# Kernel tuning notes

Measured on AMD Instinct MI355X. Metric: run time of the kernel, lower is better.

The kernel has to match this reference:

```python
import jax, jax.numpy as jnp
import numpy as np

H = 10          # MPC horizon
DT = 0.1
MAX_V = 0.22
MAX_W = 2.8
N_RAYS = 36
LR_INNER = 0.2
N_ITERS = 15
B = 16384


def setup_inputs() -> dict:
    key = jax.random.key(0)
    ks = jax.random.split(key, 8)
    initial_state = jax.random.normal(ks[0], (B, 3), jnp.float32)
    scan_data = jax.random.uniform(ks[1], (B, N_RAYS), jnp.float32)
    target_pos = jax.random.normal(ks[2], (B, 2), jnp.float32)
    w_dist = jax.random.uniform(ks[3], (B, 1), jnp.float32)
    w_obs = jax.random.uniform(ks[4], (B, 1), jnp.float32)
    w_angle = jax.random.uniform(ks[5], (B, 1), jnp.float32)
    w_rv = jax.random.uniform(ks[6], (B, 1), jnp.float32)
    w_rw = jax.random.uniform(ks[7], (B, 1), jnp.float32)
    return {"initial_state": initial_state, "scan_data": scan_data,
            "target_pos": target_pos, "w_dist": w_dist, "w_obs": w_obs,
            "w_angle": w_angle, "w_rv": w_rv, "w_rw": w_rw}


def _rollout_cost(action_seq, initial_state, obstacles, target_pos,
                  w_dist, w_obs, w_angle, w_rv, w_rw):
    # action_seq: [B,H,2]; obstacles: [B,36,2]
    wd, wo, wa, wv, ww = (w.reshape(-1) for w in (w_dist, w_obs, w_angle, w_rv, w_rw))

    def step(carry, a_t):  # a_t: [B,2]
        state, cost = carry
        v = (jnp.tanh(a_t[:, 0]) + 1.0) * 0.5 * MAX_V
        w = jnp.tanh(a_t[:, 1]) * MAX_W
        x = state[:, 0] + v * jnp.cos(state[:, 2]) * DT
        y = state[:, 1] + v * jnp.sin(state[:, 2]) * DT
        yaw = state[:, 2] + w * DT
        state = jnp.stack([x, y, yaw], axis=1)
        pos = state[:, :2]
        dist_to_goal = jnp.linalg.norm(pos - target_pos, axis=1)
        tdir = target_pos - pos
        tang = jnp.arctan2(tdir[:, 1], tdir[:, 0])
        aerr = jnp.arctan2(jnp.sin(tang - yaw), jnp.cos(tang - yaw))
        d_obs = jnp.linalg.norm(pos[:, None, :] - obstacles, axis=2)  # [B,36]
        min_d = jnp.min(d_obs, axis=1)
        coll = jnp.maximum(0.4 - min_d, 0.0) ** 2
        cost = cost + (dist_to_goal ** 2 * wd * 10.0
                       + aerr ** 2 * wa * 5.0
                       + coll ** 2 * wo * 100.0
                       + v ** 2 * wv * 1.0
                       + w ** 2 * ww * 0.1)
        return (state, cost), None

    bsz = initial_state.shape[0]
    init = (initial_state, jnp.zeros((bsz,), initial_state.dtype))
    (_, cost), _ = jax.lax.scan(step, init, jnp.swapaxes(action_seq, 0, 1))
    return cost.mean()


def _mpc_forward(initial_state, scan_data, target_pos,
                 w_dist, w_obs, w_angle, w_rv, w_rw):
    bsz = initial_state.shape[0]
    angles = jnp.linspace(0.0, 2.0 * jnp.pi, N_RAYS).astype(scan_data.dtype)
    obstacles = jnp.stack([scan_data * jnp.cos(angles),
                           scan_data * jnp.sin(angles)], axis=2)  # [B,36,2]
    action_seq = jnp.zeros((bsz, H, 2), initial_state.dtype)
    cost_grad = jax.grad(_rollout_cost, argnums=0)
    for _ in range(N_ITERS):
        g = cost_grad(action_seq, initial_state, obstacles, target_pos,
                      w_dist, w_obs, w_angle, w_rv, w_rw)
        action_seq = action_seq - LR_INNER * g
    a0 = action_seq[:, 0, :]
    v = (jnp.tanh(a0[:, 0]) + 1.0) * 0.5 * MAX_V
    w = jnp.tanh(a0[:, 1]) * MAX_W
    return jnp.stack([v, w], axis=1)  # [B,2]


def reference(initial_state, scan_data, target_pos,
              w_dist, w_obs, w_angle, w_rv, w_rw):
    return _mpc_forward(initial_state, scan_data, target_pos,
                        w_dist, w_obs, w_angle, w_rv, w_rw)
```

## Files before the change

### kernel.cpp

```cpp
#include <hip/hip_runtime.h>

#define H 10
#define NIT 15
#define NPAIR 9

typedef float v2f __attribute__((ext_vector_type(2)));

__device__ __forceinline__ float rcp_fast(float x) { return __builtin_amdgcn_rcpf(x); }
__device__ __forceinline__ float rsq_fast(float x) { return __builtin_amdgcn_rsqf(x); }
__device__ __forceinline__ unsigned umin2(unsigned a, unsigned b) { return a < b ? a : b; }

__device__ __forceinline__ float fast_atan2f(float y, float x) {
    float ax = fabsf(x), ay = fabsf(y);
    float mx = fmaxf(ax, ay), mn = fminf(ax, ay);
    float z = mn * rcp_fast(mx);
    float z2 = z * z;
    float p = fmaf(z2, -0.01172120f, 0.05265332f);
    p = fmaf(z2, p, -0.11643287f);
    p = fmaf(z2, p, 0.19354346f);
    p = fmaf(z2, p, -0.33262347f);
    p = fmaf(z2, p, 0.99997726f);
    p = p * z;
    p = (ay > ax) ? (1.5707964f - p) : p;
    p = (x < 0.0f) ? (3.1415927f - p) : p;
    return copysignf(p, y);
}

__global__ __launch_bounds__(256) void mpc_kernel(
    const float* __restrict__ init_state,
    const float* __restrict__ scan,
    const float* __restrict__ target,
    const float* __restrict__ wdp, const float* __restrict__ wop,
    const float* __restrict__ wap, const float* __restrict__ wvp,
    const float* __restrict__ wwp,
    float* __restrict__ out, int B)
{
    constexpr float DTc  = 0.1f;
    constexpr float MAXV = 0.22f;
    constexpr float MAXW = 2.8f;
    constexpr float LRB  = 0.2f / 16384.0f;

    __shared__ v2f s_obs[64][37];

    const int tid  = threadIdx.x;
    const int g    = blockIdx.x * 256 + tid;
    const int b    = g >> 2;
    const int sub  = tid & 3;
    const int rpar = sub & 1;
    const int tpar = (sub >> 1) & 1;
    const int e    = tid >> 2;
    if (b >= B) return;

    v2f oxp[NPAIR], oyp[NPAIR];
    #pragma unroll
    for (int j = 0; j < NPAIR; ++j) {
        int rA = rpar + 4 * j;
        int rB = rA + 2;
        float angA = (float)rA * 0.17951958020513104f;
        float angB = (float)rB * 0.17951958020513104f;
        float sA, cA, sB, cB;
        __sincosf(angA, &sA, &cA);
        __sincosf(angB, &sB, &cB);
        float dA = scan[b * 36 + rA];
        float dB = scan[b * 36 + rB];
        oxp[j] = (v2f){dA * cA, dB * cB};
        oyp[j] = (v2f){dA * sA, dB * sB};
        float wx = tpar ? oxp[j].y : oxp[j].x;
        float wy = tpar ? oyp[j].y : oyp[j].x;
        s_obs[e][sub + 4 * j] = (v2f){wx, wy};
    }
    __syncthreads();

    const float x0   = init_state[b * 3 + 0];
    const float y0   = init_state[b * 3 + 1];
    const float yaw0 = init_state[b * 3 + 2];
    const float tx   = target[b * 2 + 0];
    const float ty   = target[b * 2 + 1];
    const float wd2 = wdp[b] * 20.0f;
    const float wo  = wop[b] * 100.0f;
    const float wa2 = wap[b] * 10.0f;
    const float wv2 = wvp[b] * 2.0f;
    const float ww2 = wwp[b] * 0.2f;

    float c0, s0;
    __sincosf(yaw0, &s0, &c0);

    float a[H][2];
    #pragma unroll
    for (int t = 0; t < H; ++t) { a[t][0] = 0.0f; a[t][1] = 0.0f; }

    for (int it = 0; it < NIT; ++it) {
        float vv[H], wl[H];
        #pragma unroll
        for (int t = 0; t < H; ++t) {
            float a0 = a[t][0], a1 = a[t][1];
            float t0 = a0 * fmaf(a0 * a0, -(1.0f / 3.0f), 1.0f);
            float t1 = a1 * fmaf(a1 * a1, -(1.0f / 3.0f), 1.0f);
            vv[t] = fmaf(t0, 0.5f * MAXV, 0.5f * MAXV);
            wl[t] = t1 * MAXW;
        }

        float cv[H], sv[H];
        float sx5[5] = {0}, sy5[5] = {0};
        float ca5[5] = {0}, sa5[5] = {0};
        float x = x0, y = y0, c = c0, s = s0;
        #pragma unroll
        for (int t = 0; t < H; ++t) {
            cv[t] = c; sv[t] = s;
            float v = vv[t], w = wl[t];
            x = fmaf(v * c, DTc, x);
            y = fmaf(v * s, DTc, y);
            float z  = w * DTc;
            float z2 = z * z;
            float sz = z * fmaf(z2, -0.16666667f, 1.0f);
            float cz = fmaf(z2, -0.5f, 1.0f);
            float cn = fmaf(c, cz, -s * sz);
            float sn = fmaf(s, cz,  c * sz);
            c = cn; s = sn;
            bool mine = ((t & 1) == tpar);
            int k = t >> 1;
            sx5[k] = mine ? x : sx5[k];
            sy5[k] = mine ? y : sy5[k];
            ca5[k] = mine ? c : ca5[k];
            sa5[k] = mine ? s : sa5[k];
        }

        float pgxE[5], pgxO[5], pgyE[5], pgyO[5], pcaE[5], pcaO[5];
        #pragma unroll
        for (int k = 0; k < 5; ++k) {
            const float xp = sx5[k], yp = sy5[k];
            const float cA = ca5[k], sA = sa5[k];

            float dx = tx - xp, dy = ty - yp;
            float nn = fmaf(dy, cA, -dx * sA);
            float dd = fmaf(dx, cA,  dy * sA);
            float aerr = fast_atan2f(nn, dd);
            float ca = wa2 * aerr;
            float r2 = fmaf(dx, dx, dy * dy);
            float cr = ca * rcp_fast(r2);
            float gx = fmaf(-wd2, dx,  cr * dy);
            float gy = fmaf(-wd2, dy, -cr * dx);

            v2f xp2 = (v2f){xp, xp}, yp2 = (v2f){yp, yp};
            unsigned mm[NPAIR];
            #pragma unroll
            for (int j = 0; j < NPAIR; ++j) {
                v2f ddx = xp2 - oxp[j];
                v2f ddy = yp2 - oyp[j];
                v2f d2v = ddx * ddx + ddy * ddy;
                unsigned ua = (__builtin_bit_cast(unsigned, d2v.x) & ~63u) | (unsigned)(rpar + 4 * j);
                unsigned ub = (__builtin_bit_cast(unsigned, d2v.y) & ~63u) | (unsigned)(rpar + 4 * j + 2);
                mm[j] = umin2(ua, ub);
            }
            unsigned q0 = umin2(mm[0], mm[1]);
            unsigned q1 = umin2(mm[2], mm[3]);
            unsigned q2 = umin2(mm[4], mm[5]);
            unsigned q3 = umin2(mm[6], mm[7]);
            unsigned best = umin2(umin2(umin2(q0, q1), umin2(q2, q3)), mm[8]);
            unsigned ob = (unsigned)__shfl_xor((int)best, 1);
            best = umin2(best, ob);
            int ray = (int)(best & 63u);
            v2f obs = s_obs[e][ray];
            float bdx = xp - obs.x;
            float bdy = yp - obs.y;
            float d2m = fmaf(bdx, bdx, bdy * bdy);
            float rin  = rsq_fast(d2m);
            float mind = d2m * rin;
            float m    = fmaxf(0.4f - mind, 0.0f);
            float sg   = -4.0f * wo * m * m * m * rin;
            float pgx = fmaf(sg, bdx, gx);
            float pgy = fmaf(sg, bdy, gy);

            float ogx = __shfl_xor(pgx, 2);
            float ogy = __shfl_xor(pgy, 2);
            float oca = __shfl_xor(ca, 2);
            pgxE[k] = tpar ? ogx : pgx;  pgxO[k] = tpar ? pgx : ogx;
            pgyE[k] = tpar ? ogy : pgy;  pgyO[k] = tpar ? pgy : ogy;
            pcaE[k] = tpar ? oca : ca;   pcaO[k] = tpar ? ca  : oca;
        }

        float Gx = 0.0f, Gy = 0.0f, Gyaw = 0.0f;
        #pragma unroll
        for (int t = H - 1; t >= 0; --t) {
            const int k = t >> 1;
            float pgx = (t & 1) ? pgxO[k] : pgxE[k];
            float pgy = (t & 1) ? pgyO[k] : pgyE[k];
            float pca = (t & 1) ? pcaO[k] : pcaE[k];
            float gx   = Gx + pgx;
            float gy   = Gy + pgy;
            float gyaw = Gyaw - pca;
            const float cy = cv[t], sy = sv[t], v = vv[t], w = wl[t];

            float gv = fmaf(gx, cy, gy * sy) * DTc + wv2 * v;
            float gw = fmaf(ww2, w, gyaw * DTc);
            float tv = a[t][0];
            float tw = a[t][1];
            a[t][0] = fmaf(-LRB, gv * (0.5f * MAXV) * fmaf(-tv, tv, 1.0f), a[t][0]);
            a[t][1] = fmaf(-LRB, gw * MAXW * fmaf(-tw, tw, 1.0f), a[t][1]);

            Gyaw = fmaf((gy * cy - gx * sy) * v, DTc, gyaw);
            Gx = gx;
            Gy = gy;
        }
    }

    if (sub == 0) {
        float v = (tanhf(a[0][0]) + 1.0f) * 0.5f * MAXV;
        float w = tanhf(a[0][1]) * MAXW;
        out[b * 2 + 0] = v;
        out[b * 2 + 1] = w;
    }
}

extern "C" void kernel_launch(void* const* d_in, const int* in_sizes, int n_in,
                              void* d_out, int out_size, void* d_ws, size_t ws_size,
                              hipStream_t stream) {
    const float* init_state = (const float*)d_in[0];
    const float* scan       = (const float*)d_in[1];
    const float* target     = (const float*)d_in[2];
    const float* wd         = (const float*)d_in[3];
    const float* wo         = (const float*)d_in[4];
    const float* wa         = (const float*)d_in[5];
    const float* wv         = (const float*)d_in[6];
    const float* ww         = (const float*)d_in[7];
    int B = in_sizes[0] / 3;
    int threads = B * 4;
    int blocks = (threads + 255) / 256;
    mpc_kernel<<<blocks, 256, 0, stream>>>(init_state, scan, target, wd, wo, wa, wv, ww,
                                           (float*)d_out, B);
}
```

Before: 37.57 us.

## Track nearest obstacle offsets in registers and use DPP quad swizzles

Replaces the packed-index argmin plus shared-memory obstacle lookup with a running min that carries the dx/dy of the nearest obstacle in registers, removing the LDS table, the block barrier and the recomputation of the distance. Cross-lane exchanges (xor 1 and xor 2 within a quad) switch from __shfl_xor, which goes through LDS permute, to DPP quad_perm moves. The per-ray compare-and-select chain becomes serial and adds three extra lane exchanges per step. Tie-breaking may differ slightly from the old packed comparison.

```diff
diff --git a/kernel.cpp b/kernel.cpp
--- a/kernel.cpp
+++ b/kernel.cpp
@@ -8,7 +8,15 @@
 
 __device__ __forceinline__ float rcp_fast(float x) { return __builtin_amdgcn_rcpf(x); }
 __device__ __forceinline__ float rsq_fast(float x) { return __builtin_amdgcn_rsqf(x); }
-__device__ __forceinline__ unsigned umin2(unsigned a, unsigned b) { return a < b ? a : b; }
+
+template <int CTRL>
+__device__ __forceinline__ float dpp_qp(float x) {
+    int i = __builtin_bit_cast(int, x);
+    int r = __builtin_amdgcn_update_dpp(i, i, CTRL, 0xF, 0xF, true);
+    return __builtin_bit_cast(float, r);
+}
+#define DPP_XOR1 0xB1
+#define DPP_XOR2 0x4E
 
 __device__ __forceinline__ float fast_atan2f(float y, float x) {
     float ax = fabsf(x), ay = fabsf(y);
@@ -40,15 +48,12 @@
     constexpr float MAXW = 2.8f;
     constexpr float LRB  = 0.2f / 16384.0f;
 
-    __shared__ v2f s_obs[64][37];
-
     const int tid  = threadIdx.x;
     const int g    = blockIdx.x * 256 + tid;
     const int b    = g >> 2;
     const int sub  = tid & 3;
     const int rpar = sub & 1;
     const int tpar = (sub >> 1) & 1;
-    const int e    = tid >> 2;
     if (b >= B) return;
 
     v2f oxp[NPAIR], oyp[NPAIR];
@@ -65,11 +70,7 @@
         float dB = scan[b * 36 + rB];
         oxp[j] = (v2f){dA * cA, dB * cB};
         oyp[j] = (v2f){dA * sA, dB * sB};
-        float wx = tpar ? oxp[j].y : oxp[j].x;
-        float wy = tpar ? oyp[j].y : oyp[j].x;
-        s_obs[e][sub + 4 * j] = (v2f){wx, wy};
     }
-    __syncthreads();
 
     const float x0   = init_state[b * 3 + 0];
     const float y0   = init_state[b * 3 + 1];
@@ -142,38 +143,40 @@
             float gy = fmaf(-wd2, dy, -cr * dx);
 
             v2f xp2 = (v2f){xp, xp}, yp2 = (v2f){yp, yp};
-            unsigned mm[NPAIR];
+            float bestd2 = 1e30f, bdx = 0.0f, bdy = 0.0f;
             #pragma unroll
             for (int j = 0; j < NPAIR; ++j) {
                 v2f ddx = xp2 - oxp[j];
                 v2f ddy = yp2 - oyp[j];
                 v2f d2v = ddx * ddx + ddy * ddy;
-                unsigned ua = (__builtin_bit_cast(unsigned, d2v.x) & ~63u) | (unsigned)(rpar + 4 * j);
-                unsigned ub = (__builtin_bit_cast(unsigned, d2v.y) & ~63u) | (unsigned)(rpar + 4 * j + 2);
-                mm[j] = umin2(ua, ub);
+                bool c0b = d2v.x < bestd2;
+                bestd2 = fminf(d2v.x, bestd2);
+                bdx = c0b ? ddx.x : bdx;
+                bdy = c0b ? ddy.x : bdy;
+                bool c1b = d2v.y < bestd2;
+                bestd2 = fminf(d2v.y, bestd2);
+                bdx = c1b ? ddx.y : bdx;
+                bdy = c1b ? ddy.y : bdy;
             }
-            unsigned q0 = umin2(mm[0], mm[1]);
-            unsigned q1 = umin2(mm[2], mm[3]);
-            unsigned q2 = umin2(mm[4], mm[5]);
-            unsigned q3 = umin2(mm[6], mm[7]);
-            unsigned best = umin2(umin2(umin2(q0, q1), umin2(q2, q3)), mm[8]);
-            unsigned ob = (unsigned)__shfl_xor((int)best, 1);
-            best = umin2(best, ob);
-            int ray = (int)(best & 63u);
-            v2f obs = s_obs[e][ray];
-            float bdx = xp - obs.x;
-            float bdy = yp - obs.y;
-            float d2m = fmaf(bdx, bdx, bdy * bdy);
-            float rin  = rsq_fast(d2m);
-            float mind = d2m * rin;
+            {
+                float od2 = dpp_qp<DPP_XOR1>(bestd2);
+                float odx = dpp_qp<DPP_XOR1>(bdx);
+                float ody = dpp_qp<DPP_XOR1>(bdy);
+                bool cb = od2 < bestd2;
+                bestd2 = fminf(od2, bestd2);
+                bdx = cb ? odx : bdx;
+                bdy = cb ? ody : bdy;
+            }
+            float rin  = rsq_fast(bestd2);
+            float mind = bestd2 * rin;
             float m    = fmaxf(0.4f - mind, 0.0f);
             float sg   = -4.0f * wo * m * m * m * rin;
             float pgx = fmaf(sg, bdx, gx);
             float pgy = fmaf(sg, bdy, gy);
 
-            float ogx = __shfl_xor(pgx, 2);
-            float ogy = __shfl_xor(pgy, 2);
-            float oca = __shfl_xor(ca, 2);
+            float ogx = dpp_qp<DPP_XOR2>(pgx);
+            float ogy = dpp_qp<DPP_XOR2>(pgy);
+            float oca = dpp_qp<DPP_XOR2>(ca);
             pgxE[k] = tpar ? ogx : pgx;  pgxO[k] = tpar ? pgx : ogx;
             pgyE[k] = tpar ? ogy : pgy;  pgyO[k] = tpar ? pgy : ogy;
             pcaE[k] = tpar ? oca : ca;   pcaO[k] = tpar ? ca  : oca;
```

Measured after the change: 40.53 us. +7.9%, slower.
